# Performance work log

Measured on AMD Instinct MI355X. Metric: run time of the kernel, lower is better.

The kernel has to match this reference:

```python
import jax, jax.numpy as jnp
import numpy as np

DIM = 256
HEADS = 8


def setup_inputs() -> dict:
    key = jax.random.key(0)
    ks = jax.random.split(key, 12)
    B, N, L, C, H = 2, 1024, 4096, DIM, HEADS
    s = C ** -0.5
    inp = {
        "query": jax.random.normal(ks[0], (B, N, C), jnp.float32),
        "key": jax.random.normal(ks[1], (B, L, C), jnp.float32),
        "value": jax.random.normal(ks[2], (B, L, C), jnp.float32),
        "key_padding_mask": jnp.zeros((B, L), jnp.bool_),
        "hw_lvl": 1,
        # nn.Linear weights, stored as (out, in) like torch
        "Wq": jax.random.normal(ks[3], (C, C), jnp.float32) * s,
        "Wk": jax.random.normal(ks[4], (C, C), jnp.float32) * s,
        "Wv": jax.random.normal(ks[5], (C, C), jnp.float32) * s,
        "Wp": jax.random.normal(ks[6], (C, C), jnp.float32) * s,
        "bp": jax.random.normal(ks[7], (C,), jnp.float32) * 0.02,
        "W1": jax.random.normal(ks[8], (H, H), jnp.float32) * H ** -0.5,
        "b1": jax.random.normal(ks[9], (H,), jnp.float32) * 0.02,
        "W2": jax.random.normal(ks[10], (1, H), jnp.float32) * H ** -0.5,
        "b2": jax.random.normal(ks[11], (1,), jnp.float32) * 0.02,
    }
    return inp


def reference(query, key, value, key_padding_mask, hw_lvl,
              Wq, Wk, Wv, Wp, bp, W1, b1, W2, b2):
    # key_padding_mask and hw_lvl are accepted but unused by the original module.
    B, N, C = query.shape
    L = key.shape[1]
    H = W1.shape[0]
    D = C // H
    scale = D ** -0.5

    q = (query @ Wq.T).reshape(B, N, H, D)  # bnhd
    k = (key @ Wk.T).reshape(B, L, H, D)    # blhd
    v = (value @ Wv.T).reshape(B, L, H, D)  # blhd

    # raw attention scores [B, H, N, L]
    attn = jnp.einsum("bnhd,blhd->bhnl", q, k) * scale

    # per-score tiny MLP over the head axis -> mask [B, N, L, 1]
    scores_nlh = attn.transpose(0, 2, 3, 1)  # [B, N, L, H]
    new_feats = jax.nn.relu(scores_nlh @ W1.T + b1)
    mask = jax.nn.relu(new_feats @ W2.T + b2)  # [B, N, L, 1]

    a = jax.nn.softmax(attn, axis=-1)  # dropout p=0 -> identity
    x = jnp.einsum("bhnl,blhd->bnhd", a, v).reshape(B, N, C)
    x = x @ Wp.T + bp
    return x, mask
```

## Files before the change

### kernel.cpp

```cpp
#include <hip/hip_runtime.h>

typedef unsigned short u16;
typedef unsigned int u32;
typedef __attribute__((ext_vector_type(8))) short bf16x8;
typedef __attribute__((ext_vector_type(4))) short bf16x4;
typedef __attribute__((ext_vector_type(4))) float f32x4;

#define QK_SCALE 0.17677669529663687f

__device__ inline float bf2f(u16 h) {
    u32 u = ((u32)h) << 16; float f; __builtin_memcpy(&f, &u, 4); return f;
}
__device__ inline u16 f2bf(float f) {
    u32 u; __builtin_memcpy(&u, &f, 4);
    u = u + 0x7fffu + ((u >> 16) & 1u);
    return (u16)(u >> 16);
}

__global__ __launch_bounds__(256) void cvt_all_kernel(
    const float* __restrict__ q, const float* __restrict__ k,
    const float* __restrict__ v,
    const float* __restrict__ Wq, const float* __restrict__ Wk,
    const float* __restrict__ Wv, const float* __restrict__ Wp,
    u16* __restrict__ qf, u16* __restrict__ kf, u16* __restrict__ vf,
    u16* __restrict__ wqb, u16* __restrict__ wkb, u16* __restrict__ wvb,
    u16* __restrict__ wpb)
{
    const int bx = blockIdx.x;
    const float* src; u16* dst; int base;
    if (bx < 256)       { src = q;  dst = qf;  base = bx; }
    else if (bx < 1280) { src = k;  dst = kf;  base = bx - 256; }
    else if (bx < 2304) { src = v;  dst = vf;  base = bx - 1280; }
    else if (bx < 2336) { src = Wq; dst = wqb; base = bx - 2304; }
    else if (bx < 2368) { src = Wk; dst = wkb; base = bx - 2336; }
    else if (bx < 2400) { src = Wv; dst = wvb; base = bx - 2368; }
    else                { src = Wp; dst = wpb; base = bx - 2400; }
    const int i = base * 2048 + threadIdx.x * 8;
    const f32x4 a = *(const f32x4*)(src + i);
    const f32x4 b = *(const f32x4*)(src + i + 4);
    bf16x8 o;
#pragma unroll
    for (int j = 0; j < 4; ++j) {
        o[j]     = (short)f2bf(a[j]);
        o[j + 4] = (short)f2bf(b[j]);
    }
    *(bf16x8*)(dst + i) = o;
}

__global__ __launch_bounds__(256) void proj_kernel(
    const u16* __restrict__ qf, const u16* __restrict__ kf,
    const u16* __restrict__ vf,
    const u16* __restrict__ wqb, const u16* __restrict__ wkb,
    const u16* __restrict__ wvb,
    u16* __restrict__ qb, u16* __restrict__ kb, u16* __restrict__ vt)
{
    const int bx = blockIdx.x;
    const u16 *X, *W; u16* outb; int m0, mode;
    if (bx < 128)      { X = qf; W = wqb; outb = qb; m0 = bx * 16; mode = 2; }
    else if (bx < 640) { X = kf; W = wkb; outb = kb; m0 = (bx - 128) * 16; mode = 0; }
    else               { X = vf; W = wvb; outb = vt; m0 = (bx - 640) * 16; mode = 1; }

    const int lane = threadIdx.x & 63;
    const int w = threadIdx.x >> 6;
    const int r = lane & 15, g = lane >> 4;
    const int c0 = blockIdx.y * 64 + w * 16;
    const u16* ap = X + (long)(m0 + r) * 256 + g * 8;
    const u16* bp = W + (long)(c0 + r) * 256 + g * 8;

    bf16x8 af[8], bf[8];
#pragma unroll
    for (int ks = 0; ks < 8; ++ks) af[ks] = *(const bf16x8*)(ap + ks * 32);
#pragma unroll
    for (int ks = 0; ks < 8; ++ks) bf[ks] = *(const bf16x8*)(bp + ks * 32);

    f32x4 acc = {0.f, 0.f, 0.f, 0.f};
#pragma unroll
    for (int ks = 0; ks < 8; ++ks)
        acc = __builtin_amdgcn_mfma_f32_16x16x32_bf16(af[ks], bf[ks], acc, 0, 0, 0);

    const int c = c0 + r;
    if (mode == 1) {
        const int m_ = m0 + g * 4;
        const int b = m_ >> 12, l = m_ & 4095;
        bf16x4 pk;
#pragma unroll
        for (int j = 0; j < 4; ++j) pk[j] = (short)f2bf(acc[j]);
        *(bf16x4*)(vt + (long)b * 1048576 + (long)(l >> 2) * 1024 + c * 4) = pk;
    } else {
#pragma unroll
        for (int j = 0; j < 4; ++j) {
            const int m = m0 + g * 4 + j;
            if (mode == 2) outb[(long)m * 256 + c] = f2bf(acc[j] * QK_SCALE);
            else           outb[(long)m * 256 + c] = f2bf(acc[j]);
        }
    }
}

__global__ __launch_bounds__(256, 2) void attn_split_kernel(
    const u16* __restrict__ qb, const u16* __restrict__ kb,
    const u16* __restrict__ vt,
    const float* __restrict__ W1, const float* __restrict__ b1,
    const float* __restrict__ W2, const float* __restrict__ b2,
    u16* __restrict__ Opart, float* __restrict__ stats,
    float* __restrict__ out)
{
    __shared__ float ored[4][8][2][4][16][4];
    __shared__ float rs[4][8][16];

    const int tid = threadIdx.x;
    const int w = tid >> 6, lane = tid & 63;
    const int r = lane & 15, g = lane >> 4;
    const int bi = blockIdx.y;
    const int n0 = blockIdx.x * 16;
    const int cz = blockIdx.z;

    float w1r[64], b1r[8], w2r[8];
#pragma unroll
    for (int i = 0; i < 64; ++i) w1r[i] = W1[i];
#pragma unroll
    for (int i = 0; i < 8; ++i) { b1r[i] = b1[i]; w2r[i] = W2[i]; }
    const float b2r = b2[0];

    bf16x8 qh[8];
    const long qbase = (long)(bi * 1024 + n0 + r) * 256 + g * 8;
#pragma unroll
    for (int h = 0; h < 8; ++h)
        qh[h] = *(const bf16x8*)(qb + qbase + h * 32);

    f32x4 oacc[8][2];
#pragma unroll
    for (int h = 0; h < 8; ++h)
#pragma unroll
        for (int c = 0; c < 2; ++c) oacc[h][c] = (f32x4){0.f, 0.f, 0.f, 0.f};
    float rsum[8];
#pragma unroll
    for (int h = 0; h < 8; ++h) rsum[h] = 0.f;

    bf16x8 kf[8];
    {
        const long kbb = (long)(bi * 4096 + cz * 512 + w * 16 + r) * 256 + g * 8;
#pragma unroll
        for (int h = 0; h < 8; ++h)
            kf[h] = *(const bf16x8*)(kb + kbb + h * 32);
    }

    for (int t = 0; t < 8; ++t) {
        const int l0 = cz * 512 + t * 64;

        bf16x4 vf[8][2];
        {
            const u16* vb = vt + (long)bi * 1048576 +
                            (long)((l0 >> 2) + w * 4 + g) * 1024;
#pragma unroll
            for (int h = 0; h < 8; ++h)
#pragma unroll
                for (int c = 0; c < 2; ++c)
                    vf[h][c] = *(const bf16x4*)(vb + (h * 32 + c * 16 + r) * 4);
        }

        f32x4 so[8], ss[8];
#pragma unroll
        for (int h = 0; h < 8; ++h) {
            f32x4 z = {0.f, 0.f, 0.f, 0.f};
            so[h] = __builtin_amdgcn_mfma_f32_16x16x32_bf16(qh[h], kf[h], z, 0, 0, 0);
        }
#pragma unroll
        for (int h = 0; h < 8; ++h) {
            f32x4 z = {0.f, 0.f, 0.f, 0.f};
            ss[h] = __builtin_amdgcn_mfma_f32_16x16x32_bf16(kf[h], qh[h], z, 0, 0, 0);
        }

        if (t < 7) {
            const long kbb = (long)(bi * 4096 + l0 + 64 + w * 16 + r) * 256 + g * 8;
#pragma unroll
            for (int h = 0; h < 8; ++h)
                kf[h] = *(const bf16x8*)(kb + kbb + h * 32);
        }

        {
            float* mout = out + 524288l + (long)(bi * 1024 + n0) * 4096
                        + l0 + w * 16 + r;
#pragma unroll
            for (int j = 0; j < 4; ++j) {
                float mv = b2r;
#pragma unroll
                for (int f = 0; f < 8; ++f) {
                    float ft = b1r[f];
#pragma unroll
                    for (int h = 0; h < 8; ++h)
                        ft = fmaf(so[h][j], w1r[f * 8 + h], ft);
                    mv = fmaf(fmaxf(ft, 0.f), w2r[f], mv);
                }
                mout[(long)(g * 4 + j) * 4096] = fmaxf(mv, 0.f);
            }
        }

        bf16x4 pa[8];
#pragma unroll
        for (int h = 0; h < 8; ++h) {
            float e0 = __expf(ss[h][0] - 8.f);
            float e1 = __expf(ss[h][1] - 8.f);
            float e2 = __expf(ss[h][2] - 8.f);
            float e3 = __expf(ss[h][3] - 8.f);
            rsum[h] += (e0 + e1) + (e2 + e3);
            u32 u0, u1, u2, u3;
            __builtin_memcpy(&u0, &e0, 4); __builtin_memcpy(&u1, &e1, 4);
            __builtin_memcpy(&u2, &e2, 4); __builtin_memcpy(&u3, &e3, 4);
            u32 lohi[2];
            lohi[0] = (u0 >> 16) | (u1 & 0xFFFF0000u);
            lohi[1] = (u2 >> 16) | (u3 & 0xFFFF0000u);
            __builtin_memcpy(&pa[h], lohi, 8);
        }

#pragma unroll
        for (int h = 0; h < 8; ++h)
#pragma unroll
            for (int c = 0; c < 2; ++c)
                oacc[h][c] = __builtin_amdgcn_mfma_f32_16x16x16bf16_1k(
                    pa[h], vf[h][c], oacc[h][c], 0, 0, 0);
    }

#pragma unroll
    for (int h = 0; h < 8; ++h)
#pragma unroll
        for (int c = 0; c < 2; ++c)
            *(f32x4*)&ored[w][h][c][g][r][0] = oacc[h][c];
#pragma unroll
    for (int h = 0; h < 8; ++h) {
        float v = rsum[h];
        v += __shfl_xor(v, 16);
        v += __shfl_xor(v, 32);
        if (g == 0) rs[w][h][r] = v;
    }
    __syncthreads();

    if (tid < 128) {
        const int h = tid >> 4, n = tid & 15;
        stats[((long)(bi * 8 + cz) * 8 + h) * 1024 + n0 + n] =
            rs[0][h][n] + rs[1][h][n] + rs[2][h][n] + rs[3][h][n];
    }
    {
        const int h = tid >> 5, c = (tid >> 4) & 1, rr = tid & 15;
#pragma unroll
        for (int g2 = 0; g2 < 4; ++g2)
#pragma unroll
            for (int j = 0; j < 4; ++j) {
                const float val = ored[0][h][c][g2][rr][j] + ored[1][h][c][g2][rr][j]
                                + ored[2][h][c][g2][rr][j] + ored[3][h][c][g2][rr][j];
                const int n = g2 * 4 + j;
                Opart[((long)(bi * 8 + cz) * 1024 + n0 + n) * 256
                      + h * 32 + c * 16 + rr] = f2bf(val);
            }
    }
}

__global__ __launch_bounds__(256) void reduce_kernel(
    const u16* __restrict__ Opart, const float* __restrict__ stats,
    const u16* __restrict__ wpb, const float* __restrict__ bp,
    float* __restrict__ out)
{
    __shared__ __align__(16) u16 xt[16 * 272];
    const int tid = threadIdx.x;
    const int w = tid >> 6, lane = tid & 63;
    const int r = lane & 15, g = lane >> 4;
    const int bi = blockIdx.y, n0 = blockIdx.x * 16;
    const int n = tid >> 4, cg = tid & 15, h = cg >> 1;

    float S = 0.f, O[16];
#pragma unroll
    for (int k = 0; k < 16; ++k) O[k] = 0.f;
#pragma unroll
    for (int c = 0; c < 8; ++c) {
        S += stats[((long)(bi * 8 + c) * 8 + h) * 1024 + n0 + n];
        const bf16x8* op = (const bf16x8*)(Opart +
            ((long)(bi * 8 + c) * 1024 + n0 + n) * 256 + cg * 16);
        bf16x8 v0 = op[0], v1 = op[1];
#pragma unroll
        for (int k = 0; k < 8; ++k) {
            O[k]     += bf2f((u16)v0[k]);
            O[k + 8] += bf2f((u16)v1[k]);
        }
    }
    const float inv = 1.f / S;
#pragma unroll
    for (int k = 0; k < 16; ++k)
        xt[n * 272 + cg * 16 + k] = f2bf(O[k] * inv);
    __syncthreads();

    bf16x8 a8[8];
#pragma unroll
    for (int ks = 0; ks < 8; ++ks)
        a8[ks] = *(const bf16x8*)(&xt[r * 272 + ks * 32 + g * 8]);
#pragma unroll
    for (int kblk = 0; kblk < 4; ++kblk) {
        const int cp0 = (w + kblk * 4) * 16;
        f32x4 acc = {0.f, 0.f, 0.f, 0.f};
#pragma unroll
        for (int ks = 0; ks < 8; ++ks) {
            bf16x8 wb = *(const bf16x8*)(wpb + (long)(cp0 + r) * 256 + ks * 32 + g * 8);
            acc = __builtin_amdgcn_mfma_f32_16x16x32_bf16(a8[ks], wb, acc, 0, 0, 0);
        }
        const int cp = cp0 + r;
        const float bpv = bp[cp];
#pragma unroll
        for (int j = 0; j < 4; ++j) {
            const int nn = g * 4 + j;
            out[(long)(bi * 1024 + n0 + nn) * 256 + cp] = acc[j] + bpv;
        }
    }
}

extern "C" void kernel_launch(void* const* d_in, const int* in_sizes, int n_in,
                              void* d_out, int out_size, void* d_ws, size_t ws_size,
                              hipStream_t stream)
{
    const float* query = (const float*)d_in[0];
    const float* key   = (const float*)d_in[1];
    const float* value = (const float*)d_in[2];
    const float* Wq = (const float*)d_in[5];
    const float* Wk = (const float*)d_in[6];
    const float* Wv = (const float*)d_in[7];
    const float* Wp = (const float*)d_in[8];
    const float* bp = (const float*)d_in[9];
    const float* W1 = (const float*)d_in[10];
    const float* b1 = (const float*)d_in[11];
    const float* W2 = (const float*)d_in[12];
    const float* b2 = (const float*)d_in[13];

    u16* qb    = (u16*)d_ws;
    u16* kb    = qb + 524288;
    u16* vtp   = kb + 2097152;
    u16* wpb   = vtp + 2097152;
    u16* Opart = wpb + 65536;
    u16* kfb   = Opart;
    u16* vfb   = Opart + 2097152;
    float* stats = (float*)(Opart + 4194304);
    u16* qfb   = (u16*)(stats + 131072);
    u16* wqb   = qfb + 524288;
    u16* wkb   = wqb + 65536;
    u16* wvb   = wkb + 65536;
    float* out = (float*)d_out;

    cvt_all_kernel<<<2432, 256, 0, stream>>>(
        query, key, value, Wq, Wk, Wv, Wp,
        qfb, kfb, vfb, wqb, wkb, wvb, wpb);
    proj_kernel<<<dim3(1152, 4), 256, 0, stream>>>(
        qfb, kfb, vfb, wqb, wkb, wvb, qb, kb, vtp);
    attn_split_kernel<<<dim3(64, 2, 8), 256, 0, stream>>>(
        qb, kb, vtp, W1, b1, W2, b2, Opart, stats, out);
    reduce_kernel<<<dim3(64, 2), 256, 0, stream>>>(Opart, stats, wpb, bp, out);
}
```

Before: 119.4 us.

## Raise attention kernel occupancy: halve LDS reduction buffer, packed-fp32 mask MLP

Raises the launch bound on the split attention kernel from 2 to 4 blocks per SM. To support that, the cross-wave output reduction buffer in shared memory is halved by running the reduction in two phases with an extra barrier. The per-score head MLP is rewritten with 2-wide float vectors so the compiler can emit packed FMA/max instructions. The higher occupancy target caps registers per thread, which may cause spills given the large register arrays (w1r, qh, oacc, kf).

```diff
diff --git a/kernel.cpp b/kernel.cpp
--- a/kernel.cpp
+++ b/kernel.cpp
@@ -5,6 +5,7 @@
 typedef __attribute__((ext_vector_type(8))) short bf16x8;
 typedef __attribute__((ext_vector_type(4))) short bf16x4;
 typedef __attribute__((ext_vector_type(4))) float f32x4;
+typedef __attribute__((ext_vector_type(2))) float f32x2;
 
 #define QK_SCALE 0.17677669529663687f
 
@@ -96,7 +97,7 @@
     }
 }
 
-__global__ __launch_bounds__(256, 2) void attn_split_kernel(
+__global__ __launch_bounds__(256, 4) void attn_split_kernel(
     const u16* __restrict__ qb, const u16* __restrict__ kb,
     const u16* __restrict__ vt,
     const float* __restrict__ W1, const float* __restrict__ b1,
@@ -104,7 +105,7 @@
     u16* __restrict__ Opart, float* __restrict__ stats,
     float* __restrict__ out)
 {
-    __shared__ float ored[4][8][2][4][16][4];
+    __shared__ float ored[4][8][2][2][16][4];
     __shared__ float rs[4][8][16];
 
     const int tid = threadIdx.x;
@@ -181,17 +182,26 @@
             float* mout = out + 524288l + (long)(bi * 1024 + n0) * 4096
                         + l0 + w * 16 + r;
 #pragma unroll
-            for (int j = 0; j < 4; ++j) {
-                float mv = b2r;
+            for (int jp = 0; jp < 2; ++jp) {
+                f32x2 s2[8];
+#pragma unroll
+                for (int h = 0; h < 8; ++h)
+                    s2[h] = (f32x2){so[h][jp * 2], so[h][jp * 2 + 1]};
+                f32x2 mv = {b2r, b2r};
 #pragma unroll
                 for (int f = 0; f < 8; ++f) {
-                    float ft = b1r[f];
-#pragma unroll
-                    for (int h = 0; h < 8; ++h)
-                        ft = fmaf(so[h][j], w1r[f * 8 + h], ft);
-                    mv = fmaf(fmaxf(ft, 0.f), w2r[f], mv);
+                    f32x2 ft = {b1r[f], b1r[f]};
+#pragma unroll
+                    for (int h = 0; h < 8; ++h) {
+                        const float wv = w1r[f * 8 + h];
+                        ft = __builtin_elementwise_fma(s2[h], (f32x2){wv, wv}, ft);
+                    }
+                    ft = __builtin_elementwise_max(ft, (f32x2){0.f, 0.f});
+                    mv = __builtin_elementwise_fma(ft, (f32x2){w2r[f], w2r[f]}, mv);
                 }
-                mout[(long)(g * 4 + j) * 4096] = fmaxf(mv, 0.f);
+                mv = __builtin_elementwise_max(mv, (f32x2){0.f, 0.f});
+                mout[(long)(g * 4 + jp * 2) * 4096]     = mv[0];
+                mout[(long)(g * 4 + jp * 2 + 1) * 4096] = mv[1];
             }
         }
 
@@ -221,36 +231,42 @@
     }
 
 #pragma unroll
-    for (int h = 0; h < 8; ++h)
-#pragma unroll
-        for (int c = 0; c < 2; ++c)
-            *(f32x4*)&ored[w][h][c][g][r][0] = oacc[h][c];
-#pragma unroll
     for (int h = 0; h < 8; ++h) {
         float v = rsum[h];
         v += __shfl_xor(v, 16);
         v += __shfl_xor(v, 32);
         if (g == 0) rs[w][h][r] = v;
     }
-    __syncthreads();
-
-    if (tid < 128) {
-        const int h = tid >> 4, n = tid & 15;
-        stats[((long)(bi * 8 + cz) * 8 + h) * 1024 + n0 + n] =
-            rs[0][h][n] + rs[1][h][n] + rs[2][h][n] + rs[3][h][n];
-    }
-    {
-        const int h = tid >> 5, c = (tid >> 4) & 1, rr = tid & 15;
-#pragma unroll
-        for (int g2 = 0; g2 < 4; ++g2)
-#pragma unroll
-            for (int j = 0; j < 4; ++j) {
-                const float val = ored[0][h][c][g2][rr][j] + ored[1][h][c][g2][rr][j]
-                                + ored[2][h][c][g2][rr][j] + ored[3][h][c][g2][rr][j];
-                const int n = g2 * 4 + j;
-                Opart[((long)(bi * 8 + cz) * 1024 + n0 + n) * 256
-                      + h * 32 + c * 16 + rr] = f2bf(val);
-            }
+#pragma unroll
+    for (int ph = 0; ph < 2; ++ph) {
+        if ((g >> 1) == ph) {
+#pragma unroll
+            for (int h = 0; h < 8; ++h)
+#pragma unroll
+                for (int c = 0; c < 2; ++c)
+                    *(f32x4*)&ored[w][h][c][g & 1][r][0] = oacc[h][c];
+        }
+        __syncthreads();
+        if (ph == 0 && tid < 128) {
+            const int h = tid >> 4, n = tid & 15;
+            stats[((long)(bi * 8 + cz) * 8 + h) * 1024 + n0 + n] =
+                rs[0][h][n] + rs[1][h][n] + rs[2][h][n] + rs[3][h][n];
+        }
+        {
+            const int h = tid >> 5, c = (tid >> 4) & 1, rr = tid & 15;
+#pragma unroll
+            for (int g2 = 0; g2 < 2; ++g2)
+#pragma unroll
+                for (int j = 0; j < 4; ++j) {
+                    const float val =
+                        ored[0][h][c][g2][rr][j] + ored[1][h][c][g2][rr][j] +
+                        ored[2][h][c][g2][rr][j] + ored[3][h][c][g2][rr][j];
+                    const int n = (ph * 2 + g2) * 4 + j;
+                    Opart[((long)(bi * 8 + cz) * 1024 + n0 + n) * 256
+                          + h * 32 + c * 16 + rr] = f2bf(val);
+                }
+        }
+        if (ph == 0) __syncthreads();
     }
 }
 
```

New measurement: 341.4 us. 186% more time.
